# Kernel optimization log

Measured on AMD Instinct MI355X. Metric: run time of the kernel, lower is better.

## Reference

```python
import jax, jax.numpy as jnp
import numpy as np
from jax import lax

DIM = 128
HEADS = 4
HEAD_DIM = DIM // HEADS          # 32
SR = 2
BN_EPS = 1e-5


def setup_inputs() -> dict:
    key = jax.random.key(0)
    ks = jax.random.split(key, 16)
    B, N, C = 8, 3136, DIM
    H = W = 56
    Nkv = (H // SR) * (W // SR)  # 784
    s = 0.05
    inp = {
        "x": jax.random.normal(ks[0], (B, N, C), jnp.float32),
        "relative_pos": jax.random.normal(ks[1], (HEADS, N, Nkv), jnp.float32),
        "Wq": jax.random.normal(ks[2], (C, C), jnp.float32) * s,
        "bq": jnp.zeros((C,), jnp.float32),
        "Wk": jax.random.normal(ks[3], (C, C), jnp.float32) * s,
        "bk": jnp.zeros((C,), jnp.float32),
        "Wv": jax.random.normal(ks[4], (C, C), jnp.float32) * s,
        "bv": jnp.zeros((C,), jnp.float32),
        "conv_w": jax.random.normal(ks[5], (C, 1, SR, SR), jnp.float32) * s,  # depthwise OIHW
        "conv_b": jnp.zeros((C,), jnp.float32),
        "bn_gamma": jnp.ones((C,), jnp.float32),
        "bn_beta": jnp.zeros((C,), jnp.float32),
        "bn_mean": jax.random.normal(ks[6], (C,), jnp.float32) * 0.1,
        "bn_var": jax.random.uniform(ks[7], (C,), jnp.float32, 0.5, 1.5),
        "Wp": jax.random.normal(ks[8], (C, C), jnp.float32) * s,
        "bp": jnp.zeros((C,), jnp.float32),
        "H": H,
        "W": W,
    }
    return inp


def reference(x, relative_pos, Wq, bq, Wk, bk, Wv, bv, conv_w, conv_b,
              bn_gamma, bn_beta, bn_mean, bn_var, Wp, bp, H, W):
    B, N, C = x.shape
    scale = HEAD_DIM ** -0.5

    # q: (B, heads, N, head_dim)
    q = (x @ Wq + bq).reshape(B, N, HEADS, HEAD_DIM).transpose(0, 2, 1, 3)

    # spatial reduction: depthwise conv stride SR + BatchNorm (eval, running stats)
    x_img = x.transpose(0, 2, 1).reshape(B, C, H, W)
    y = lax.conv_general_dilated(
        x_img, conv_w, window_strides=(SR, SR), padding="VALID",
        feature_group_count=C,
        dimension_numbers=("NCHW", "OIHW", "NCHW")) + conv_b[None, :, None, None]
    inv = bn_gamma * lax.rsqrt(bn_var + BN_EPS)
    y = y * inv[None, :, None, None] + (bn_beta - bn_mean * inv)[None, :, None, None]
    x_ = y.reshape(B, C, -1).transpose(0, 2, 1)  # (B, Nkv, C)
    Nkv = x_.shape[1]

    k = (x_ @ Wk + bk).reshape(B, Nkv, HEADS, HEAD_DIM).transpose(0, 2, 1, 3)
    v = (x_ @ Wv + bv).reshape(B, Nkv, HEADS, HEAD_DIM).transpose(0, 2, 1, 3)

    attn = jnp.einsum("bhnd,bhmd->bhnm", q, k) * scale + relative_pos[None]
    attn = jax.nn.softmax(attn, axis=-1)
    out = jnp.einsum("bhnm,bhmd->bhnd", attn, v)
    out = out.transpose(0, 2, 1, 3).reshape(B, N, C)
    return out @ Wp + bp
```

## Files before the change

kernel.cpp:

```cpp
#include <hip/hip_runtime.h>
#include <hip/hip_bf16.h>

#define BATCH 8
#define NQ 3136
#define CDIM 128
#define NHEAD 4
#define HD 32
#define NKV 784
#define HIMG 56
#define SCALE 0.17677669529663687f

typedef __attribute__((ext_vector_type(8))) short bf8_t;
typedef __attribute__((ext_vector_type(4))) float f4_t;

using bf16 = __hip_bfloat16;
using u16  = unsigned short;

static __device__ __forceinline__ float b2f(bf16 v){ return __bfloat162float(v); }
static __device__ __forceinline__ bf16  f2b(float v){ return __float2bfloat16(v); }
static __device__ __forceinline__ short f2s(float v){
  union { bf16 b; short s; } u; u.b = f2b(v); return u.s;
}
static __device__ __forceinline__ float u16f(u16 x){
  union { u16 u; bf16 b; } c; c.u = x; return b2f(c.b);
}
static __device__ __forceinline__ float ld1(const void* p, size_t i, int f){
  return f ? b2f(((const bf16*)p)[i]) : ((const float*)p)[i];
}
static __device__ __forceinline__ float4 ld4f(const void* p, size_t i, int f){
  if (f){
    ushort4 u = *(const ushort4*)((const bf16*)p + i);
    return make_float4(u16f(u.x), u16f(u.y), u16f(u.z), u16f(u.w));
  }
  return *(const float4*)((const float*)p + i);
}
static __device__ __forceinline__ bf8_t ld8(const void* p, size_t i, int f){
  if (f) return *(const bf8_t*)((const bf16*)p + i);
  const float* fp = (const float*)p + i;
  float4 a = *(const float4*)fp;
  float4 b = *(const float4*)(fp + 4);
  bf8_t r;
  r[0]=f2s(a.x); r[1]=f2s(a.y); r[2]=f2s(a.z); r[3]=f2s(a.w);
  r[4]=f2s(b.x); r[5]=f2s(b.y); r[6]=f2s(b.z); r[7]=f2s(b.w);
  return r;
}
static __device__ __forceinline__ int detect_flag(const void* var_raw){
  const u16* h = (const u16*)var_raw;
  int lane = threadIdx.x & 63;
  bool ok = true;
  #pragma unroll
  for (int t = 0; t < 2; t++){
    union { u16 u; bf16 b; } cv; cv.u = h[lane + 64*t];
    float v = b2f(cv.b);
    ok = ok && (v > 0.3f) && (v < 1.7f);
  }
  return (__ballot(ok) == ~0ull) ? 1 : 0;
}

static __device__ __forceinline__ void mfma_row(
    const bf8_t a[4], const bf16* __restrict__ Wt, int m, int g, f4_t acc[8])
{
  #pragma unroll
  for (int ct = 0; ct < 8; ct++){
    f4_t c = {0.f,0.f,0.f,0.f};
    const bf16* bp = Wt + (size_t)(ct*16 + m)*CDIM + 8*g;
    #pragma unroll
    for (int ks = 0; ks < 4; ks++){
      bf8_t b = *(const bf8_t*)(bp + 32*ks);
      c = __builtin_amdgcn_mfma_f32_16x16x32_bf16(a[ks], b, c, 0,0,0);
    }
    acc[ct] = c;
  }
}

__global__ __launch_bounds__(256) void prep_kernel(
    const void* __restrict__ Wq, const void* __restrict__ Wk,
    const void* __restrict__ Wv, const void* __restrict__ Wp,
    const void* __restrict__ var, const void* __restrict__ cw,
    const void* __restrict__ cb, const void* __restrict__ gam,
    const void* __restrict__ bet, const void* __restrict__ mea,
    const void* __restrict__ bq, const void* __restrict__ bk,
    const void* __restrict__ bv, const void* __restrict__ bp,
    bf16* __restrict__ Wqt, bf16* __restrict__ Wkt,
    bf16* __restrict__ Wvt, bf16* __restrict__ Wpt,
    bf16* __restrict__ bqs, bf16* __restrict__ bks,
    bf16* __restrict__ bvs, bf16* __restrict__ bps,
    float* __restrict__ cwf, float* __restrict__ inv, float* __restrict__ shift2)
{
  int f = detect_flag(var);
  int idx = blockIdx.x*256 + threadIdx.x;
  int mat = idx >> 14;
  int e   = idx & 16383;
  int o = e >> 7, i = e & 127;
  const void* src; bf16* dst; float s = 1.f;
  if      (mat == 0){ src = Wq; dst = Wqt; s = SCALE; }
  else if (mat == 1){ src = Wk; dst = Wkt; }
  else if (mat == 2){ src = Wv; dst = Wvt; }
  else              { src = Wp; dst = Wpt; }
  dst[e] = f2b(ld1(src, (size_t)i*128 + o, f) * s);

  if (blockIdx.x == 0){
    int t = threadIdx.x;
    { int e2 = t;       cwf[(e2&3)*128 + (e2>>2)] = ld1(cw, e2, f); }
    { int e2 = t + 256; cwf[(e2&3)*128 + (e2>>2)] = ld1(cw, e2, f); }
    if (t < 128){
      bqs[t] = f2b(ld1(bq, t, f) * SCALE);
      bks[t] = f2b(ld1(bk, t, f));
      bvs[t] = f2b(ld1(bv, t, f));
      bps[t] = f2b(ld1(bp, t, f));
      float iv = ld1(gam, t, f) * rsqrtf(ld1(var, t, f) + 1e-5f);
      inv[t] = iv;
      shift2[t] = ld1(bet, t, f) - ld1(mea, t, f) * iv + ld1(cb, t, f) * iv;
    }
  }
}

__global__ __launch_bounds__(256) void fat_kernel(
    const void* __restrict__ x, const void* __restrict__ var,
    const float* __restrict__ cwf, const float* __restrict__ inv,
    const float* __restrict__ shift2, bf16* __restrict__ xr,
    const bf16* __restrict__ Wqt, const bf16* __restrict__ bqs,
    bf16* __restrict__ qbf,
    const void* __restrict__ rel, bf16* __restrict__ relb, int qblk)
{
  int f = detect_flag(var);
  if (blockIdx.x < 784){
    int idx = blockIdx.x*256 + threadIdx.x;
    int c0 = (idx & 31)*4;
    int t  = idx >> 5;
    int b  = t / NKV;
    int kv = t - b*NKV;
    int i = kv/28, j = kv - i*28;
    size_t base = (size_t)(b*NQ + 2*i*HIMG + 2*j)*CDIM + c0;
    float4 t0 = ld4f(x, base, f);
    float4 t1 = ld4f(x, base + CDIM, f);
    float4 t2 = ld4f(x, base + HIMG*CDIM, f);
    float4 t3 = ld4f(x, base + HIMG*CDIM + CDIM, f);
    float4 w0 = *(const float4*)(cwf + c0);
    float4 w1 = *(const float4*)(cwf + 128 + c0);
    float4 w2 = *(const float4*)(cwf + 256 + c0);
    float4 w3 = *(const float4*)(cwf + 384 + c0);
    float4 iv4 = *(const float4*)(inv + c0);
    float4 sh4 = *(const float4*)(shift2 + c0);
    union { u16 h[4]; uint2 u; } pk;
    float a;
    a = t0.x*w0.x + t1.x*w1.x + t2.x*w2.x + t3.x*w3.x; pk.h[0] = (u16)f2s(a*iv4.x + sh4.x);
    a = t0.y*w0.y + t1.y*w1.y + t2.y*w2.y + t3.y*w3.y; pk.h[1] = (u16)f2s(a*iv4.y + sh4.y);
    a = t0.z*w0.z + t1.z*w1.z + t2.z*w2.z + t3.z*w3.z; pk.h[2] = (u16)f2s(a*iv4.z + sh4.z);
    a = t0.w*w0.w + t1.w*w1.w + t2.w*w2.w + t3.w*w3.w; pk.h[3] = (u16)f2s(a*iv4.w + sh4.w);
    *(uint2*)(xr + (size_t)t*CDIM + c0) = pk.u;
  } else if ((int)blockIdx.x < 784 + qblk){
    int wave = threadIdx.x >> 6, lane = threadIdx.x & 63;
    int m = lane & 15, g = lane >> 4;
    int task = (blockIdx.x - 784)*4 + wave;
    int row0 = task*16;
    bf8_t a[4];
    #pragma unroll
    for (int ks = 0; ks < 4; ks++)
      a[ks] = ld8(x, (size_t)(row0 + m)*CDIM + 8*g + 32*ks, f);
    f4_t acc[8];
    mfma_row(a, Wqt, m, g, acc);
    #pragma unroll
    for (int ct = 0; ct < 8; ct++){
      int col = ct*16 + m;
      float bv = b2f(bqs[col]);
      #pragma unroll
      for (int r = 0; r < 4; r++)
        qbf[(size_t)(row0 + 4*g + r)*CDIM + col] = f2b(acc[ct][r] + bv);
    }
  } else {
    if (f) return;
    int bi = blockIdx.x - 784 - qblk;
    size_t gid = ((size_t)bi*256 + threadIdx.x)*8;
    const float* fp = (const float*)rel + gid;
    float4 a  = *(const float4*)fp;
    float4 b4 = *(const float4*)(fp + 4);
    union { u16 hh[8]; uint4 u4; } pk;
    pk.hh[0]=(u16)f2s(a.x);  pk.hh[1]=(u16)f2s(a.y);
    pk.hh[2]=(u16)f2s(a.z);  pk.hh[3]=(u16)f2s(a.w);
    pk.hh[4]=(u16)f2s(b4.x); pk.hh[5]=(u16)f2s(b4.y);
    pk.hh[6]=(u16)f2s(b4.z); pk.hh[7]=(u16)f2s(b4.w);
    *(uint4*)(relb + gid) = pk.u4;
  }
}

__global__ __launch_bounds__(256) void kv_kernel(
    const bf16* __restrict__ xr,
    const bf16* __restrict__ Wkt, const bf16* __restrict__ Wvt,
    const bf16* __restrict__ bks, const bf16* __restrict__ bvs,
    bf16* __restrict__ kbf, bf16* __restrict__ vtb)
{
  int wave = threadIdx.x >> 6, lane = threadIdx.x & 63;
  int m = lane & 15, g = lane >> 4;
  bool isK = blockIdx.x < 98;
  int bx = isK ? blockIdx.x : blockIdx.x - 98;
  int row0 = (bx*4 + wave)*16;
  bf8_t a[4];
  #pragma unroll
  for (int ks = 0; ks < 4; ks++)
    a[ks] = *(const bf8_t*)(xr + (size_t)(row0 + m)*CDIM + 8*g + 32*ks);
  f4_t acc[8];
  mfma_row(a, isK ? Wkt : Wvt, m, g, acc);

  if (isK){
    #pragma unroll
    for (int ct = 0; ct < 8; ct++){
      int col = ct*16 + m;
      float bv = b2f(bks[col]);
      #pragma unroll
      for (int r = 0; r < 4; r++)
        kbf[(size_t)(row0 + 4*g + r)*CDIM + col] = f2b(acc[ct][r] + bv);
    }
  } else {
    int b   = row0 / NKV;
    int kv0 = row0 - b*NKV + 4*g;
    #pragma unroll
    for (int ct = 0; ct < 8; ct++){
      int col = ct*16 + m;
      float bv = b2f(bvs[col]);
      int h = col >> 5, d = col & 31;
      union { bf16 hh[4]; uint2 u; } pk;
      #pragma unroll
      for (int r = 0; r < 4; r++) pk.hh[r] = f2b(acc[ct][r] + bv);
      *(uint2*)(vtb + (size_t)((b*NHEAD + h)*HD + d)*NKV + kv0) = pk.u;
    }
  }
}

template<int RM> struct RelV { using T = float4; };
template<> struct RelV<1> { using T = uint2; };

template<int RM>
static __device__ __forceinline__ typename RelV<RM>::T relld(const void* relp, int off){
  if constexpr (RM == 1) return *(const uint2*)((const bf16*)relp + off);
  else                   return *(const float4*)((const float*)relp + off);
}
template<int RM>
static __device__ __forceinline__ float relget(const typename RelV<RM>::T& v, int r){
  if constexpr (RM == 1){
    union { uint2 u; u16 h[4]; } c; c.u = v;
    return u16f(c.h[r]);
  } else {
    return r == 0 ? v.x : (r == 1 ? v.y : (r == 2 ? v.z : v.w));
  }
}
template<int RM>
static __device__ __forceinline__ void ldrel8(
    typename RelV<RM>::T rl[8], const void* relp, int off){
  #pragma unroll
  for (int t = 0; t < 8; t++) rl[t] = relld<RM>(relp, off + 16*t);
}

template<int RM>
static __device__ __forceinline__ void chunk128(
    int kv0, const typename RelV<RM>::T rl[8],
    const bf16* __restrict__ kbase, const bf16* __restrict__ vb0,
    const bf16* __restrict__ vb1, bf16* __restrict__ pl, int m, int g,
    bf8_t q8, float& m_run, float& l_run, f4_t& O0, f4_t& O1)
{
  f4_t s[8];
  #pragma unroll
  for (int t = 0; t < 8; t++){
    bf8_t k8 = *(const bf8_t*)(kbase + (size_t)(kv0 + t*16)*CDIM);
    f4_t z = {0.f,0.f,0.f,0.f};
    s[t] = __builtin_amdgcn_mfma_f32_16x16x32_bf16(k8, q8, z, 0,0,0);
  }
  bf8_t v0[4], v1[4];
  #pragma unroll
  for (int ks = 0; ks < 4; ks++){
    v0[ks] = *(const bf8_t*)(vb0 + kv0 + ks*32 + 8*g);
    v1[ks] = *(const bf8_t*)(vb1 + kv0 + ks*32 + 8*g);
  }
  #pragma unroll
  for (int t = 0; t < 8; t++)
    #pragma unroll
    for (int r = 0; r < 4; r++)
      s[t][r] += relget<RM>(rl[t], r);
  float vmax = s[0][0];
  #pragma unroll
  for (int t = 0; t < 8; t++)
    #pragma unroll
    for (int r = 0; r < 4; r++)
      if (t + r > 0) vmax = fmaxf(vmax, s[t][r]);
  vmax = fmaxf(vmax, __shfl_xor(vmax, 16, 64));
  vmax = fmaxf(vmax, __shfl_xor(vmax, 32, 64));
  float mn = fmaxf(m_run, vmax);
  float al = __expf(m_run - mn);
  m_run = mn;
  l_run *= al;
  #pragma unroll
  for (int r = 0; r < 4; r++){ O0[r] *= al; O1[r] *= al; }
  float lsum = 0.f;
  #pragma unroll
  for (int t = 0; t < 8; t++){
    union { u16 h[4]; uint2 u; } pk;
    #pragma unroll
    for (int r = 0; r < 4; r++){
      float p = __expf(s[t][r] - m_run);
      lsum += p;
      pk.h[r] = (u16)f2s(p);
    }
    *(uint2*)(pl + m*136 + t*16 + 4*g) = pk.u;
  }
  l_run += lsum;
  #pragma unroll
  for (int ks = 0; ks < 4; ks++){
    bf8_t a8 = *(const bf8_t*)(pl + m*136 + ks*32 + 8*g);
    O0 = __builtin_amdgcn_mfma_f32_16x16x32_bf16(v0[ks], a8, O0, 0,0,0);
    O1 = __builtin_amdgcn_mfma_f32_16x16x32_bf16(v1[ks], a8, O1, 0,0,0);
  }
}

template<int RM>
static __device__ __forceinline__ void attn_run(
    const void* __restrict__ relp, const bf16* __restrict__ kbase,
    const bf16* __restrict__ vb0, const bf16* __restrict__ vb1,
    bf16* __restrict__ pl, int m, int g,
    bf8_t q8, float& m_run, float& l_run, f4_t& O0, f4_t& O1)
{
  using RT = typename RelV<RM>::T;
  RT rlA[8], rlB[8], rtv;
  ldrel8<RM>(rlA, relp, 4*g);
  #pragma unroll 1
  for (int cc = 0; cc < 3; cc++){
    int kv0 = cc*256;
    ldrel8<RM>(rlB, relp, kv0 + 128 + 4*g);
    chunk128<RM>(kv0, rlA, kbase, vb0, vb1, pl, m, g, q8, m_run, l_run, O0, O1);
    if (cc < 2) ldrel8<RM>(rlA, relp, kv0 + 256 + 4*g);
    else        rtv = relld<RM>(relp, 768 + 4*g);
    chunk128<RM>(kv0 + 128, rlB, kbase, vb0, vb1, pl, m, g, q8, m_run, l_run, O0, O1);
  }
  {
    bf8_t k8 = *(const bf8_t*)(kbase + (size_t)768*CDIM);
    f4_t z = {0.f,0.f,0.f,0.f};
    f4_t s1 = __builtin_amdgcn_mfma_f32_16x16x32_bf16(k8, q8, z, 0,0,0);
    #pragma unroll
    for (int r = 0; r < 4; r++) s1[r] += relget<RM>(rtv, r);
    float vmax = fmaxf(fmaxf(s1[0], s1[1]), fmaxf(s1[2], s1[3]));
    vmax = fmaxf(vmax, __shfl_xor(vmax, 16, 64));
    vmax = fmaxf(vmax, __shfl_xor(vmax, 32, 64));
    float mn = fmaxf(m_run, vmax);
    float al = __expf(m_run - mn);
    m_run = mn;
    l_run *= al;
    #pragma unroll
    for (int r = 0; r < 4; r++){ O0[r] *= al; O1[r] *= al; }
    union { u16 h[4]; uint2 u; } pk;
    float lsum = 0.f;
    #pragma unroll
    for (int r = 0; r < 4; r++){
      float p = __expf(s1[r] - m_run);
      lsum += p;
      pk.h[r] = (u16)f2s(p);
    }
    *(uint2*)(pl + m*136 + 4*g) = pk.u;
    l_run += lsum;
    bf8_t a8, v0, v1;
    if (g >= 2){
      bf8_t z8 = {0,0,0,0,0,0,0,0};
      a8 = z8; v0 = z8; v1 = z8;
    } else {
      a8 = *(const bf8_t*)(pl + m*136 + 8*g);
      v0 = *(const bf8_t*)(vb0 + 768 + 8*g);
      v1 = *(const bf8_t*)(vb1 + 768 + 8*g);
    }
    O0 = __builtin_amdgcn_mfma_f32_16x16x32_bf16(v0, a8, O0, 0,0,0);
    O1 = __builtin_amdgcn_mfma_f32_16x16x32_bf16(v1, a8, O1, 0,0,0);
  }
}

template<int QF, int FB>
static __device__ __forceinline__ void attn_device(
    const bf16* __restrict__ qbf, const void* __restrict__ x,
    const bf16* __restrict__ Wqt, const bf16* __restrict__ bqs,
    const bf16* __restrict__ kb, const bf16* __restrict__ vtb,
    const void* __restrict__ rel, const bf16* __restrict__ relb,
    const void* __restrict__ var,
    void* __restrict__ dout, bf16* __restrict__ obf)
{
  int f = detect_flag(var);
  int wave = threadIdx.x >> 6, lane = threadIdx.x & 63;
  int m = lane & 15, g = lane >> 4;
  int qt = blockIdx.x, h = blockIdx.y, b = blockIdx.z;
  int qrow0 = qt*64 + wave*16;

  __shared__ bf16 Plds[4][16*136];
  bf16* pl = Plds[wave];

  bf8_t q8;
  if constexpr (QF == 0){
    q8 = *(const bf8_t*)(qbf + (size_t)(b*NQ + qrow0 + m)*CDIM + h*HD + 8*g);
  } else {
    bf8_t xa[4];
    #pragma unroll
    for (int ks = 0; ks < 4; ks++)
      xa[ks] = ld8(x, (size_t)(b*NQ + qrow0 + m)*CDIM + 8*g + 32*ks, f);
    f4_t qc0 = {0.f,0.f,0.f,0.f}, qc1 = {0.f,0.f,0.f,0.f};
    const bf16* wp0 = Wqt + (size_t)(h*HD + m)*CDIM + 8*g;
    const bf16* wp1 = Wqt + (size_t)(h*HD + 16 + m)*CDIM + 8*g;
    #pragma unroll
    for (int ks = 0; ks < 4; ks++){
      bf8_t w0 = *(const bf8_t*)(wp0 + 32*ks);
      bf8_t w1 = *(const bf8_t*)(wp1 + 32*ks);
      qc0 = __builtin_amdgcn_mfma_f32_16x16x32_bf16(xa[ks], w0, qc0, 0,0,0);
      qc1 = __builtin_amdgcn_mfma_f32_16x16x32_bf16(xa[ks], w1, qc1, 0,0,0);
    }
    float bv0 = b2f(bqs[h*HD + m]);
    float bv1 = b2f(bqs[h*HD + 16 + m]);
    #pragma unroll
    for (int r = 0; r < 4; r++){
      pl[(4*g + r)*136 + m]      = f2b(qc0[r] + bv0);
      pl[(4*g + r)*136 + 16 + m] = f2b(qc1[r] + bv1);
    }
    q8 = *(const bf8_t*)(pl + m*136 + 8*g);
  }

  const bf16* kbase = kb  + (size_t)(b*NKV + m)*CDIM + h*HD + 8*g;
  const bf16* vb0   = vtb + (size_t)((b*NHEAD + h)*HD + m)*NKV;
  const bf16* vb1   = vtb + (size_t)((b*NHEAD + h)*HD + 16 + m)*NKV;
  size_t rrow = ((size_t)h*NQ + qrow0 + m)*(size_t)NKV;

  float m_run = -1e30f, l_run = 0.f;
  f4_t O0 = {0.f,0.f,0.f,0.f}, O1 = {0.f,0.f,0.f,0.f};

  if constexpr (FB == 0){
    const void* rsrc = f ? (const void*)((const bf16*)rel + rrow)
                         : (const void*)(relb + rrow);
    attn_run<1>(rsrc, kbase, vb0, vb1, pl, m, g, q8, m_run, l_run, O0, O1);
  } else {
    if (f) attn_run<1>((const void*)((const bf16*)rel + rrow), kbase, vb0, vb1,
                       pl, m, g, q8, m_run, l_run, O0, O1);
    else   attn_run<0>((const void*)((const float*)rel + rrow), kbase, vb0, vb1,
                       pl, m, g, q8, m_run, l_run, O0, O1);
  }

  l_run += __shfl_xor(l_run, 16, 64);
  l_run += __shfl_xor(l_run, 32, 64);
  float iv = 1.0f / l_run;

  union { u16 h4[4]; uint2 u; } o0, o1;
  #pragma unroll
  for (int r = 0; r < 4; r++){
    o0.h4[r] = (u16)f2s(O0[r] * iv);
    o1.h4[r] = (u16)f2s(O1[r] * iv);
  }
  *(uint2*)(pl + m*136 + 4*g)      = o0.u;
  *(uint2*)(pl + m*136 + 16 + 4*g) = o1.u;
  int r2 = lane >> 2;
  int c2 = (lane & 3)*8;
  bf8_t ov = *(const bf8_t*)(pl + r2*136 + c2);
  bf16* ob = (f ? (bf16*)dout : obf);
  *(bf8_t*)(ob + (size_t)(b*NQ + qrow0 + r2)*CDIM + h*HD + c2) = ov;
}

template<int QF>
__global__ __launch_bounds__(256) void attn_kernel(
    const bf16* __restrict__ qbf, const void* __restrict__ x,
    const bf16* __restrict__ Wqt, const bf16* __restrict__ bqs,
    const bf16* __restrict__ kb, const bf16* __restrict__ vtb,
    const void* __restrict__ rel, const bf16* __restrict__ relb,
    const void* __restrict__ var,
    void* __restrict__ dout, bf16* __restrict__ obf)
{
  attn_device<QF,0>(qbf, x, Wqt, bqs, kb, vtb, rel, relb, var, dout, obf);
}

__global__ __launch_bounds__(256) void attn_kernel_fb(
    const bf16* __restrict__ qbf, const void* __restrict__ x,
    const bf16* __restrict__ Wqt, const bf16* __restrict__ bqs,
    const bf16* __restrict__ kb, const bf16* __restrict__ vtb,
    const void* __restrict__ rel, const bf16* __restrict__ relb,
    const void* __restrict__ var,
    void* __restrict__ dout, bf16* __restrict__ obf)
{
  attn_device<1,1>(qbf, x, Wqt, bqs, kb, vtb, rel, relb, var, dout, obf);
}

__global__ __launch_bounds__(256) void proj_kernel(
    const bf16* A0, const bf16* A1, const bf16* __restrict__ Wt,
    const bf16* __restrict__ bias, void* outp, const void* __restrict__ var)
{
  int f = detect_flag(var);
  const bf16* A = f ? A0 : A1;
  int wave = threadIdx.x >> 6, lane = threadIdx.x & 63;
  int m = lane & 15, g = lane >> 4;
  int row0 = (blockIdx.x*4 + wave)*16;
  bf8_t a[4];
  #pragma unroll
  for (int ks = 0; ks < 4; ks++)
    a[ks] = *(const bf8_t*)(A + (size_t)(row0 + m)*CDIM + 8*g + 32*ks);
  f4_t acc[8];
  mfma_row(a, Wt, m, g, acc);
  #pragma unroll
  for (int ct = 0; ct < 8; ct++){
    int col = ct*16 + m;
    float bv = b2f(bias[col]);
    #pragma unroll
    for (int r = 0; r < 4; r++){
      size_t oi = (size_t)(row0 + 4*g + r)*CDIM + col;
      float v = acc[ct][r] + bv;
      if (f) ((bf16*)outp)[oi]  = f2b(v);
      else   ((float*)outp)[oi] = v;
    }
  }
}

extern "C" void kernel_launch(void* const* d_in, const int* in_sizes, int n_in,
                              void* d_out, int out_size, void* d_ws, size_t ws_size,
                              hipStream_t stream)
{
  const void* x   = d_in[0];
  const void* rel = d_in[1];
  const void* Wq  = d_in[2];
  const void* bq  = d_in[3];
  const void* Wk  = d_in[4];
  const void* bk  = d_in[5];
  const void* Wv  = d_in[6];
  const void* bv  = d_in[7];
  const void* cw  = d_in[8];
  const void* cb  = d_in[9];
  const void* gam = d_in[10];
  const void* bet = d_in[11];
  const void* mea = d_in[12];
  const void* var = d_in[13];
  const void* Wp  = d_in[14];
  const void* bp  = d_in[15];

  char* w = (char*)d_ws;
  auto alloc = [&](size_t bytes){
    char* p = w; w += (bytes + 255) & ~(size_t)255; return p;
  };
  bf16* Wqt = (bf16*)alloc(128*128*sizeof(bf16));
  bf16* Wkt = (bf16*)alloc(128*128*sizeof(bf16));
  bf16* Wvt = (bf16*)alloc(128*128*sizeof(bf16));
  bf16* Wpt = (bf16*)alloc(128*128*sizeof(bf16));
  bf16* bqs = (bf16*)alloc(128*sizeof(bf16));
  bf16* bks = (bf16*)alloc(128*sizeof(bf16));
  bf16* bvs = (bf16*)alloc(128*sizeof(bf16));
  bf16* bps = (bf16*)alloc(128*sizeof(bf16));
  float* cwf    = (float*)alloc(512*sizeof(float));
  float* inv    = (float*)alloc(128*sizeof(float));
  float* shift2 = (float*)alloc(128*sizeof(float));
  bf16* xr  = (bf16*)alloc((size_t)BATCH*NKV*CDIM*sizeof(bf16));
  bf16* kbf = (bf16*)alloc((size_t)BATCH*NKV*CDIM*sizeof(bf16));
  bf16* vtb = (bf16*)alloc((size_t)BATCH*NKV*CDIM*sizeof(bf16));
  bf16* obf = (bf16*)alloc((size_t)BATCH*NQ*CDIM*sizeof(bf16));

  size_t relb_bytes = (size_t)NHEAD*NQ*NKV*sizeof(bf16);
  bf16* relb = nullptr;
  if (((char*)d_ws + ws_size) - w >= (ptrdiff_t)(relb_bytes + 256))
    relb = (bf16*)alloc(relb_bytes);

  size_t qbf_bytes = (size_t)BATCH*NQ*CDIM*sizeof(bf16);
  bool use_q = relb &&
      ((((char*)d_ws + ws_size) - w) >= (ptrdiff_t)(qbf_bytes + 256));
  bf16* qbf = use_q ? (bf16*)alloc(qbf_bytes) : nullptr;

  int qblk = use_q ? 392 : 0;
  int rblk = relb  ? 4802 : 0;

  prep_kernel<<<256, 256, 0, stream>>>(Wq, Wk, Wv, Wp, var, cw, cb, gam, bet, mea,
                                       bq, bk, bv, bp,
                                       Wqt, Wkt, Wvt, Wpt, bqs, bks, bvs, bps,
                                       cwf, inv, shift2);
  fat_kernel<<<784 + qblk + rblk, 256, 0, stream>>>(
      x, var, cwf, inv, shift2, xr, Wqt, bqs, qbf, rel, relb, qblk);
  kv_kernel<<<196, 256, 0, stream>>>(xr, Wkt, Wvt, bks, bvs, kbf, vtb);
  dim3 ag(49, NHEAD, BATCH);
  if (relb){
    if (use_q)
      attn_kernel<0><<<ag, 256, 0, stream>>>(
          qbf, x, Wqt, bqs, kbf, vtb, rel, relb, var, d_out, obf);
    else
      attn_kernel<1><<<ag, 256, 0, stream>>>(
          qbf, x, Wqt, bqs, kbf, vtb, rel, relb, var, d_out, obf);
  } else {
    attn_kernel_fb<<<ag, 256, 0, stream>>>(
        qbf, x, Wqt, bqs, kbf, vtb, rel, relb, var, d_out, obf);
  }
  proj_kernel<<<392, 256, 0, stream>>>((const bf16*)d_out, obf, Wpt, bps, d_out, var);
}
```

Baseline: 236.8 us.

## Prefetch K and rel tiles across chunks, lazy softmax rescale, one-wave blocks

Fully unrolls the KV chunk loop and double-buffers K tiles and relative-position values, so the next chunk's loads are issued while the current chunk computes. Adds a lazy rescale: running max and output are updated only when some lane's new max exceeds the old one by more than 8. Swaps MFMA operand order so the output is in a transposed layout, written straight to global without the LDS transpose. Launches one 64-thread wave per block instead of four. These aim to hide memory latency and cut per-chunk work, at the cost of more registers and scattered scalar bf16 stores.

```diff
diff --git a/kernel.cpp b/kernel.cpp
--- a/kernel.cpp
+++ b/kernel.cpp
@@ -251,19 +251,28 @@
   for (int t = 0; t < 8; t++) rl[t] = relld<RM>(relp, off + 16*t);
 }
 
-template<int RM>
+template<int RM, int PF>
 static __device__ __forceinline__ void chunk128(
-    int kv0, const typename RelV<RM>::T rl[8],
-    const bf16* __restrict__ kbase, const bf16* __restrict__ vb0,
-    const bf16* __restrict__ vb1, bf16* __restrict__ pl, int m, int g,
-    bf8_t q8, float& m_run, float& l_run, f4_t& O0, f4_t& O1)
+    int kv0,
+    typename RelV<RM>::T rl[8], bf8_t kc[8],
+    typename RelV<RM>::T rln[8], bf8_t kn[8],
+    const void* __restrict__ relp, const bf16* __restrict__ kbase,
+    const bf16* __restrict__ vb0, const bf16* __restrict__ vb1,
+    bf16* __restrict__ pl, int m, int g, bf8_t q8,
+    float& m_run, float& l_run, f4_t& O0, f4_t& O1)
 {
   f4_t s[8];
   #pragma unroll
   for (int t = 0; t < 8; t++){
-    bf8_t k8 = *(const bf8_t*)(kbase + (size_t)(kv0 + t*16)*CDIM);
     f4_t z = {0.f,0.f,0.f,0.f};
-    s[t] = __builtin_amdgcn_mfma_f32_16x16x32_bf16(k8, q8, z, 0,0,0);
+    s[t] = __builtin_amdgcn_mfma_f32_16x16x32_bf16(kc[t], q8, z, 0,0,0);
+  }
+  if constexpr (PF == 2){
+    #pragma unroll
+    for (int t = 0; t < 8; t++)
+      kn[t] = *(const bf8_t*)(kbase + (size_t)(kv0 + 128 + t*16)*CDIM);
+  } else if constexpr (PF == 1){
+    kn[0] = *(const bf8_t*)(kbase + (size_t)768*CDIM);
   }
   bf8_t v0[4], v1[4];
   #pragma unroll
@@ -276,6 +285,8 @@
     #pragma unroll
     for (int r = 0; r < 4; r++)
       s[t][r] += relget<RM>(rl[t], r);
+  if constexpr (PF == 2) ldrel8<RM>(rln, relp, kv0 + 128 + 4*g);
+  else if constexpr (PF == 1) rln[0] = relld<RM>(relp, 768 + 4*g);
   float vmax = s[0][0];
   #pragma unroll
   for (int t = 0; t < 8; t++)
@@ -284,12 +295,17 @@
       if (t + r > 0) vmax = fmaxf(vmax, s[t][r]);
   vmax = fmaxf(vmax, __shfl_xor(vmax, 16, 64));
   vmax = fmaxf(vmax, __shfl_xor(vmax, 32, 64));
-  float mn = fmaxf(m_run, vmax);
-  float al = __expf(m_run - mn);
-  m_run = mn;
-  l_run *= al;
-  #pragma unroll
-  for (int r = 0; r < 4; r++){ O0[r] *= al; O1[r] *= al; }
+  if (!__all(vmax <= m_run + 8.f)){
+    float mn = fmaxf(m_run, vmax);
+    float al = __expf(m_run - mn);
+    m_run = mn;
+    l_run *= al;
+    float alT[4];
+    #pragma unroll
+    for (int r = 0; r < 4; r++) alT[r] = __shfl(al, 4*g + r, 64);
+    #pragma unroll
+    for (int r = 0; r < 4; r++){ O0[r] *= alT[r]; O1[r] *= alT[r]; }
+  }
   float lsum = 0.f;
   #pragma unroll
   for (int t = 0; t < 8; t++){
@@ -306,8 +322,8 @@
   #pragma unroll
   for (int ks = 0; ks < 4; ks++){
     bf8_t a8 = *(const bf8_t*)(pl + m*136 + ks*32 + 8*g);
-    O0 = __builtin_amdgcn_mfma_f32_16x16x32_bf16(v0[ks], a8, O0, 0,0,0);
-    O1 = __builtin_amdgcn_mfma_f32_16x16x32_bf16(v1[ks], a8, O1, 0,0,0);
+    O0 = __builtin_amdgcn_mfma_f32_16x16x32_bf16(a8, v0[ks], O0, 0,0,0);
+    O1 = __builtin_amdgcn_mfma_f32_16x16x32_bf16(a8, v1[ks], O1, 0,0,0);
   }
 }
 
@@ -319,32 +335,39 @@
     bf8_t q8, float& m_run, float& l_run, f4_t& O0, f4_t& O1)
 {
   using RT = typename RelV<RM>::T;
-  RT rlA[8], rlB[8], rtv;
+  RT rlA[8], rlB[8];
+  bf8_t kA[8], kB[8];
   ldrel8<RM>(rlA, relp, 4*g);
-  #pragma unroll 1
-  for (int cc = 0; cc < 3; cc++){
-    int kv0 = cc*256;
-    ldrel8<RM>(rlB, relp, kv0 + 128 + 4*g);
-    chunk128<RM>(kv0, rlA, kbase, vb0, vb1, pl, m, g, q8, m_run, l_run, O0, O1);
-    if (cc < 2) ldrel8<RM>(rlA, relp, kv0 + 256 + 4*g);
-    else        rtv = relld<RM>(relp, 768 + 4*g);
-    chunk128<RM>(kv0 + 128, rlB, kbase, vb0, vb1, pl, m, g, q8, m_run, l_run, O0, O1);
-  }
+  #pragma unroll
+  for (int t = 0; t < 8; t++)
+    kA[t] = *(const bf8_t*)(kbase + (size_t)(t*16)*CDIM);
+
+  chunk128<RM,2>(0,   rlA,kA, rlB,kB, relp,kbase,vb0,vb1,pl,m,g,q8,m_run,l_run,O0,O1);
+  chunk128<RM,2>(128, rlB,kB, rlA,kA, relp,kbase,vb0,vb1,pl,m,g,q8,m_run,l_run,O0,O1);
+  chunk128<RM,2>(256, rlA,kA, rlB,kB, relp,kbase,vb0,vb1,pl,m,g,q8,m_run,l_run,O0,O1);
+  chunk128<RM,2>(384, rlB,kB, rlA,kA, relp,kbase,vb0,vb1,pl,m,g,q8,m_run,l_run,O0,O1);
+  chunk128<RM,2>(512, rlA,kA, rlB,kB, relp,kbase,vb0,vb1,pl,m,g,q8,m_run,l_run,O0,O1);
+  chunk128<RM,1>(640, rlB,kB, rlA,kA, relp,kbase,vb0,vb1,pl,m,g,q8,m_run,l_run,O0,O1);
+
   {
-    bf8_t k8 = *(const bf8_t*)(kbase + (size_t)768*CDIM);
     f4_t z = {0.f,0.f,0.f,0.f};
-    f4_t s1 = __builtin_amdgcn_mfma_f32_16x16x32_bf16(k8, q8, z, 0,0,0);
-    #pragma unroll
-    for (int r = 0; r < 4; r++) s1[r] += relget<RM>(rtv, r);
+    f4_t s1 = __builtin_amdgcn_mfma_f32_16x16x32_bf16(kA[0], q8, z, 0,0,0);
+    #pragma unroll
+    for (int r = 0; r < 4; r++) s1[r] += relget<RM>(rlA[0], r);
     float vmax = fmaxf(fmaxf(s1[0], s1[1]), fmaxf(s1[2], s1[3]));
     vmax = fmaxf(vmax, __shfl_xor(vmax, 16, 64));
     vmax = fmaxf(vmax, __shfl_xor(vmax, 32, 64));
-    float mn = fmaxf(m_run, vmax);
-    float al = __expf(m_run - mn);
-    m_run = mn;
-    l_run *= al;
-    #pragma unroll
-    for (int r = 0; r < 4; r++){ O0[r] *= al; O1[r] *= al; }
+    if (!__all(vmax <= m_run + 8.f)){
+      float mn = fmaxf(m_run, vmax);
+      float al = __expf(m_run - mn);
+      m_run = mn;
+      l_run *= al;
+      float alT[4];
+      #pragma unroll
+      for (int r = 0; r < 4; r++) alT[r] = __shfl(al, 4*g + r, 64);
+      #pragma unroll
+      for (int r = 0; r < 4; r++){ O0[r] *= alT[r]; O1[r] *= alT[r]; }
+    }
     union { u16 h[4]; uint2 u; } pk;
     float lsum = 0.f;
     #pragma unroll
@@ -364,8 +387,8 @@
       v0 = *(const bf8_t*)(vb0 + 768 + 8*g);
       v1 = *(const bf8_t*)(vb1 + 768 + 8*g);
     }
-    O0 = __builtin_amdgcn_mfma_f32_16x16x32_bf16(v0, a8, O0, 0,0,0);
-    O1 = __builtin_amdgcn_mfma_f32_16x16x32_bf16(v1, a8, O1, 0,0,0);
+    O0 = __builtin_amdgcn_mfma_f32_16x16x32_bf16(a8, v0, O0, 0,0,0);
+    O1 = __builtin_amdgcn_mfma_f32_16x16x32_bf16(a8, v1, O1, 0,0,0);
   }
 }
 
@@ -379,13 +402,13 @@
     void* __restrict__ dout, bf16* __restrict__ obf)
 {
   int f = detect_flag(var);
-  int wave = threadIdx.x >> 6, lane = threadIdx.x & 63;
+  int lane = threadIdx.x & 63;
   int m = lane & 15, g = lane >> 4;
   int qt = blockIdx.x, h = blockIdx.y, b = blockIdx.z;
-  int qrow0 = qt*64 + wave*16;
-
-  __shared__ bf16 Plds[4][16*136];
-  bf16* pl = Plds[wave];
+  int qrow0 = qt*16;
+
+  __shared__ bf16 Plds[16*136];
+  bf16* pl = Plds;
 
   bf8_t q8;
   if constexpr (QF == 0){
@@ -436,25 +459,22 @@
 
   l_run += __shfl_xor(l_run, 16, 64);
   l_run += __shfl_xor(l_run, 32, 64);
-  float iv = 1.0f / l_run;
-
-  union { u16 h4[4]; uint2 u; } o0, o1;
+  float lT[4];
+  #pragma unroll
+  for (int r = 0; r < 4; r++) lT[r] = __shfl(l_run, 4*g + r, 64);
+
+  bf16* ob = f ? (bf16*)dout : obf;
+  size_t orow = (size_t)(b*NQ + qrow0 + 4*g);
   #pragma unroll
   for (int r = 0; r < 4; r++){
-    o0.h4[r] = (u16)f2s(O0[r] * iv);
-    o1.h4[r] = (u16)f2s(O1[r] * iv);
-  }
-  *(uint2*)(pl + m*136 + 4*g)      = o0.u;
-  *(uint2*)(pl + m*136 + 16 + 4*g) = o1.u;
-  int r2 = lane >> 2;
-  int c2 = (lane & 3)*8;
-  bf8_t ov = *(const bf8_t*)(pl + r2*136 + c2);
-  bf16* ob = (f ? (bf16*)dout : obf);
-  *(bf8_t*)(ob + (size_t)(b*NQ + qrow0 + r2)*CDIM + h*HD + c2) = ov;
+    float iv = 1.0f / lT[r];
+    ob[(orow + r)*CDIM + h*HD + m]      = f2b(O0[r] * iv);
+    ob[(orow + r)*CDIM + h*HD + 16 + m] = f2b(O1[r] * iv);
+  }
 }
 
 template<int QF>
-__global__ __launch_bounds__(256) void attn_kernel(
+__global__ __launch_bounds__(64) void attn_kernel(
     const bf16* __restrict__ qbf, const void* __restrict__ x,
     const bf16* __restrict__ Wqt, const bf16* __restrict__ bqs,
     const bf16* __restrict__ kb, const bf16* __restrict__ vtb,
@@ -465,7 +485,7 @@
   attn_device<QF,0>(qbf, x, Wqt, bqs, kb, vtb, rel, relb, var, dout, obf);
 }
 
-__global__ __launch_bounds__(256) void attn_kernel_fb(
+__global__ __launch_bounds__(64) void attn_kernel_fb(
     const bf16* __restrict__ qbf, const void* __restrict__ x,
     const bf16* __restrict__ Wqt, const bf16* __restrict__ bqs,
     const bf16* __restrict__ kb, const bf16* __restrict__ vtb,
@@ -566,16 +586,16 @@
   fat_kernel<<<784 + qblk + rblk, 256, 0, stream>>>(
       x, var, cwf, inv, shift2, xr, Wqt, bqs, qbf, rel, relb, qblk);
   kv_kernel<<<196, 256, 0, stream>>>(xr, Wkt, Wvt, bks, bvs, kbf, vtb);
-  dim3 ag(49, NHEAD, BATCH);
+  dim3 ag(196, NHEAD, BATCH);
   if (relb){
     if (use_q)
-      attn_kernel<0><<<ag, 256, 0, stream>>>(
+      attn_kernel<0><<<ag, 64, 0, stream>>>(
           qbf, x, Wqt, bqs, kbf, vtb, rel, relb, var, d_out, obf);
     else
-      attn_kernel<1><<<ag, 256, 0, stream>>>(
+      attn_kernel<1><<<ag, 64, 0, stream>>>(
           qbf, x, Wqt, bqs, kbf, vtb, rel, relb, var, d_out, obf);
   } else {
-    attn_kernel_fb<<<ag, 256, 0, stream>>>(
+    attn_kernel_fb<<<ag, 64, 0, stream>>>(
         qbf, x, Wqt, bqs, kbf, vtb, rel, relb, var, d_out, obf);
   }
   proj_kernel<<<392, 256, 0, stream>>>((const bf16*)d_out, obf, Wpt, bps, d_out, var);
```

Measured after the change: 223.3 us. 1.06x faster.
